# Optimization experiments

Hardware: AMD Instinct MI355X
Metric: run time of the kernel (lower is better)

The kernel has to match this reference:

```python
import jax, jax.numpy as jnp
import numpy as np

TOP_K = 8
NORM_TOPK_PROB = True


def setup_inputs() -> dict:
    key = jax.random.key(0)
    k1, k2 = jax.random.split(key)
    T, H, E = 16384, 4096, 64  # tokens, hidden_dim, num_experts
    hidden_states = jax.random.normal(k1, (T, H), dtype=jnp.float32)
    weight = jax.random.normal(k2, (E, H), dtype=jnp.float32) * 0.02
    return {"hidden_states": hidden_states, "weight": weight}


def reference(hidden_states, weight):
    H = weight.shape[1]
    x = hidden_states.reshape(-1, H)                      # [T, H]
    router_logits = jnp.einsum("th,eh->te", x, weight)    # [T, E]
    routing_weights = jax.nn.softmax(router_logits.astype(jnp.float32), axis=-1)
    router_top_value, router_indices = jax.lax.top_k(routing_weights, TOP_K)  # [T, k]
    if NORM_TOPK_PROB:
        router_top_value = router_top_value / jnp.sum(router_top_value, axis=-1, keepdims=True)
    router_scores = router_top_value.astype(routing_weights.dtype)
    return router_logits, router_scores, router_indices
```

## Files before the change

### kernel.cpp

```cpp
#include <hip/hip_runtime.h>
#include <math.h>

#define T_TOK  16384
#define HID    4096
#define NEXP   64
#define KSPLIT 4
#define KRANGE (HID / KSPLIT)
#define NCHUNK (KRANGE / 32)

typedef __attribute__((ext_vector_type(8))) short short8;
typedef __attribute__((ext_vector_type(4))) float float4v;

#define PART_ELEMS ((size_t)KSPLIT * T_TOK * NEXP)
#define WHALF      ((size_t)NEXP * HID)

__device__ __forceinline__ unsigned short rne_bf16(float f) {
  unsigned u = __float_as_uint(f);
  unsigned r = u + 0x7FFFu + ((u >> 16) & 1u);
  return (unsigned short)(r >> 16);
}
__device__ __forceinline__ float bf16_f(unsigned short h) {
  return __uint_as_float(((unsigned)h) << 16);
}

__global__ void w_convert3(const float* __restrict__ w,
                           unsigned short* __restrict__ wh,
                           unsigned short* __restrict__ wm,
                           unsigned short* __restrict__ wl) {
  int t = blockIdx.x * 256 + threadIdx.x;
#pragma unroll
  for (int j = 0; j < 4; ++j) {
    int idx = t + j * 65536;
    float f = w[idx];
    unsigned short h = rne_bf16(f);
    float r1 = f - bf16_f(h);
    unsigned short m = rne_bf16(r1);
    float r2 = r1 - bf16_f(m);
    wh[idx] = h; wm[idx] = m; wl[idx] = rne_bf16(r2);
  }
}

__global__ __launch_bounds__(256, 2)
void router_gemm(const float* __restrict__ x,
                 const unsigned short* __restrict__ wh,
                 const unsigned short* __restrict__ wm,
                 const unsigned short* __restrict__ wl,
                 float* __restrict__ partial) {
  const int lane = threadIdx.x & 63;
  const int wid  = threadIdx.x >> 6;
  const int W    = blockIdx.x * 4 + wid;
  const int ks   = W & (KSPLIT - 1);
  const int t0   = (W >> 2) * 32;
  const int r    = lane & 15;
  const int q    = lane >> 4;
  const int k0   = ks * KRANGE + q * 8;

  const float* pa0 = x + (size_t)(t0 + r) * HID + k0;
  const float* pa1 = pa0 + (size_t)16 * HID;
  const unsigned short* pb[3];
  pb[0] = wh + (size_t)r * HID + k0;
  pb[1] = wm + (size_t)r * HID + k0;
  pb[2] = wl + (size_t)r * HID + k0;

  float4v acc[2][4];
#pragma unroll
  for (int m = 0; m < 2; ++m)
#pragma unroll
    for (int n = 0; n < 4; ++n) acc[m][n] = (float4v)(0.f);

  float4 araw[4][2][2];
  short8 ah[2], am_[2], al[2];
  short8 Bb[2][2][3];

#define LOADA(buf, c) do {                                                   \
    const int _o = (c) * 32;                                                 \
    araw[buf][0][0] = *(const float4*)(pa0 + _o);                            \
    araw[buf][0][1] = *(const float4*)(pa0 + _o + 4);                        \
    araw[buf][1][0] = *(const float4*)(pa1 + _o);                            \
    araw[buf][1][1] = *(const float4*)(pa1 + _o + 4);                        \
  } while (0)

#define LOADB(half, c) do {                                                  \
    const int _o = (c) * 32;                                                 \
    _Pragma("unroll")                                                        \
    for (int _nl = 0; _nl < 2; ++_nl) {                                      \
      const size_t _nb = (size_t)((half) * 2 + _nl) * 16 * HID + _o;         \
      _Pragma("unroll")                                                      \
      for (int _s = 0; _s < 3; ++_s)                                         \
        Bb[half][_nl][_s] = *(const short8*)(pb[_s] + _nb);                  \
    }                                                                        \
  } while (0)

#define SPLITA(buf) do {                                                     \
    _Pragma("unroll")                                                        \
    for (int _m = 0; _m < 2; ++_m) {                                         \
      const float4 _v0 = araw[buf][_m][0], _v1 = araw[buf][_m][1];           \
      float _f[8] = {_v0.x,_v0.y,_v0.z,_v0.w,_v1.x,_v1.y,_v1.z,_v1.w};       \
      _Pragma("unroll")                                                      \
      for (int _j = 0; _j < 8; ++_j) {                                       \
        unsigned short _h = rne_bf16(_f[_j]);                                \
        float _r1 = _f[_j] - bf16_f(_h);                                     \
        unsigned short _mm = rne_bf16(_r1);                                  \
        float _r2 = _r1 - bf16_f(_mm);                                       \
        ah[_m][_j] = (short)_h; am_[_m][_j] = (short)_mm;                    \
        al[_m][_j] = (short)rne_bf16(_r2);                                   \
      }                                                                      \
    }                                                                        \
  } while (0)

#define MFMAH(half) do {                                                     \
    _Pragma("unroll")                                                        \
    for (int _nl = 0; _nl < 2; ++_nl) {                                      \
      const int _n = (half) * 2 + _nl;                                       \
      const short8 _BH = Bb[half][_nl][0];                                   \
      const short8 _BM = Bb[half][_nl][1];                                   \
      const short8 _BL = Bb[half][_nl][2];                                   \
      _Pragma("unroll")                                                      \
      for (int _m = 0; _m < 2; ++_m) {                                       \
        float4v _a = acc[_m][_n];                                            \
        _a = __builtin_amdgcn_mfma_f32_16x16x32_bf16(al[_m],  _BH, _a,0,0,0);\
        _a = __builtin_amdgcn_mfma_f32_16x16x32_bf16(ah[_m],  _BL, _a,0,0,0);\
        _a = __builtin_amdgcn_mfma_f32_16x16x32_bf16(am_[_m], _BM, _a,0,0,0);\
        _a = __builtin_amdgcn_mfma_f32_16x16x32_bf16(am_[_m], _BH, _a,0,0,0);\
        _a = __builtin_amdgcn_mfma_f32_16x16x32_bf16(ah[_m],  _BM, _a,0,0,0);\
        _a = __builtin_amdgcn_mfma_f32_16x16x32_bf16(ah[_m],  _BH, _a,0,0,0);\
        acc[_m][_n] = _a;                                                    \
      }                                                                      \
    }                                                                        \
  } while (0)

  LOADA(0, 0); LOADA(1, 1);
  LOADB(0, 0);
  for (int cc = 0; cc < NCHUNK; cc += 4) {
    if (cc + 2 < NCHUNK) LOADA(2, cc + 2);
    SPLITA(0); LOADB(1, cc);     MFMAH(0);
    LOADB(0, cc + 1);            MFMAH(1);

    if (cc + 3 < NCHUNK) LOADA(3, cc + 3);
    SPLITA(1); LOADB(1, cc + 1); MFMAH(0);
    LOADB(0, cc + 2);            MFMAH(1);

    if (cc + 4 < NCHUNK) LOADA(0, cc + 4);
    SPLITA(2); LOADB(1, cc + 2); MFMAH(0);
    LOADB(0, cc + 3);            MFMAH(1);

    if (cc + 5 < NCHUNK) LOADA(1, cc + 5);
    SPLITA(3); LOADB(1, cc + 3); MFMAH(0);
    if (cc + 4 < NCHUNK) LOADB(0, cc + 4);
    MFMAH(1);
  }
#undef LOADA
#undef LOADB
#undef SPLITA
#undef MFMAH

  float* po = partial + ((size_t)ks * T_TOK + t0) * NEXP;
#pragma unroll
  for (int m = 0; m < 2; ++m)
#pragma unroll
    for (int n = 0; n < 4; ++n)
#pragma unroll
      for (int rr = 0; rr < 4; ++rr)
        po[(size_t)(m * 16 + q * 4 + rr) * NEXP + n * 16 + r] = acc[m][n][rr];
}

__global__ __launch_bounds__(256)
void router_topk(const float* __restrict__ partial,
                 float* __restrict__ logits_out,
                 float* __restrict__ scores_out,
                 float* __restrict__ idx_out) {
  const int lane = threadIdx.x & 63;
  const int wid  = threadIdx.x >> 6;
  const int t    = blockIdx.x * 4 + wid;

  float ps[KSPLIT];
#pragma unroll
  for (int s = 0; s < KSPLIT; ++s)
    ps[s] = partial[((size_t)s * T_TOK + t) * NEXP + lane];
  float l = (ps[0] + ps[1]) + (ps[2] + ps[3]);
  logits_out[(size_t)t * NEXP + lane] = l;

  float m = l;
#pragma unroll
  for (int off = 32; off >= 1; off >>= 1)
    m = fmaxf(m, __shfl_xor(m, off, 64));
  float p = __expf(l - m);

  float v = l;
  float myscore = 0.f, myidx = 0.f, ssum = 0.f;
#pragma unroll
  for (int k = 0; k < 8; ++k) {
    float bv = v; int bi = lane;
#pragma unroll
    for (int off = 32; off >= 1; off >>= 1) {
      float ov = __shfl_xor(bv, off, 64);
      int   oi = __shfl_xor(bi, off, 64);
      if (ov > bv || (ov == bv && oi < bi)) { bv = ov; bi = oi; }
    }
    float pw = __shfl(p, bi, 64);
    ssum += pw;
    if (lane == k)  { myscore = pw; myidx = (float)bi; }
    if (lane == bi) v = -INFINITY;
  }
  if (lane < 8) {
    scores_out[(size_t)t * 8 + lane] = myscore / ssum;
    idx_out[(size_t)t * 8 + lane]    = myidx;
  }
}

extern "C" void kernel_launch(void* const* d_in, const int* in_sizes, int n_in,
                              void* d_out, int out_size, void* d_ws, size_t ws_size,
                              hipStream_t stream) {
  const float* x = (const float*)d_in[0];
  const float* w = (const float*)d_in[1];
  float* out    = (float*)d_out;
  float* logits = out;
  float* scores = out + (size_t)T_TOK * NEXP;
  float* idxo   = scores + (size_t)T_TOK * 8;

  float* partial = (float*)d_ws;
  unsigned short* wh = (unsigned short*)((char*)d_ws + PART_ELEMS * sizeof(float));
  unsigned short* wm = wh + WHALF;
  unsigned short* wl = wm + WHALF;

  hipLaunchKernelGGL(w_convert3, dim3(256), dim3(256), 0, stream, w, wh, wm, wl);
  hipLaunchKernelGGL(router_gemm, dim3(2048 / 4), dim3(256), 0, stream,
                     x, wh, wm, wl, partial);
  hipLaunchKernelGGL(router_topk, dim3(T_TOK / 4), dim3(256), 0, stream,
                     partial, logits, scores, idxo);
}
```

Baseline: 457.7 us.

## Halve per-wave token tile to 16 rows and raise GEMM occupancy

Each wave now computes 16 tokens instead of 32. That halves the accumulator and A-operand register footprint, allows launch bounds of 4 blocks per CU, and doubles the grid. The A prefetch is also deepened to three chunks ahead, and B loads are reordered ahead of the split step. The cost is that each B fragment (the three bf16 weight splits) is reused across only one M-tile instead of two, so weight-load traffic per flop doubles.

```diff
diff --git a/kernel.cpp b/kernel.cpp
--- a/kernel.cpp
+++ b/kernel.cpp
@@ -40,7 +40,7 @@
   }
 }
 
-__global__ __launch_bounds__(256, 2)
+__global__ __launch_bounds__(256, 4)
 void router_gemm(const float* __restrict__ x,
                  const unsigned short* __restrict__ wh,
                  const unsigned short* __restrict__ wm,
@@ -50,34 +50,29 @@
   const int wid  = threadIdx.x >> 6;
   const int W    = blockIdx.x * 4 + wid;
   const int ks   = W & (KSPLIT - 1);
-  const int t0   = (W >> 2) * 32;
+  const int t0   = (W >> 2) * 16;
   const int r    = lane & 15;
   const int q    = lane >> 4;
   const int k0   = ks * KRANGE + q * 8;
 
   const float* pa0 = x + (size_t)(t0 + r) * HID + k0;
-  const float* pa1 = pa0 + (size_t)16 * HID;
   const unsigned short* pb[3];
   pb[0] = wh + (size_t)r * HID + k0;
   pb[1] = wm + (size_t)r * HID + k0;
   pb[2] = wl + (size_t)r * HID + k0;
 
-  float4v acc[2][4];
-#pragma unroll
-  for (int m = 0; m < 2; ++m)
-#pragma unroll
-    for (int n = 0; n < 4; ++n) acc[m][n] = (float4v)(0.f);
-
-  float4 araw[4][2][2];
-  short8 ah[2], am_[2], al[2];
+  float4v acc[4];
+#pragma unroll
+  for (int n = 0; n < 4; ++n) acc[n] = (float4v)(0.f);
+
+  float4 araw[4][2];
+  short8 ah, am_, al;
   short8 Bb[2][2][3];
 
 #define LOADA(buf, c) do {                                                   \
     const int _o = (c) * 32;                                                 \
-    araw[buf][0][0] = *(const float4*)(pa0 + _o);                            \
-    araw[buf][0][1] = *(const float4*)(pa0 + _o + 4);                        \
-    araw[buf][1][0] = *(const float4*)(pa1 + _o);                            \
-    araw[buf][1][1] = *(const float4*)(pa1 + _o + 4);                        \
+    araw[buf][0] = *(const float4*)(pa0 + _o);                               \
+    araw[buf][1] = *(const float4*)(pa0 + _o + 4);                           \
   } while (0)
 
 #define LOADB(half, c) do {                                                  \
@@ -92,19 +87,16 @@
   } while (0)
 
 #define SPLITA(buf) do {                                                     \
+    const float4 _v0 = araw[buf][0], _v1 = araw[buf][1];                     \
+    float _f[8] = {_v0.x,_v0.y,_v0.z,_v0.w,_v1.x,_v1.y,_v1.z,_v1.w};         \
     _Pragma("unroll")                                                        \
-    for (int _m = 0; _m < 2; ++_m) {                                         \
-      const float4 _v0 = araw[buf][_m][0], _v1 = araw[buf][_m][1];           \
-      float _f[8] = {_v0.x,_v0.y,_v0.z,_v0.w,_v1.x,_v1.y,_v1.z,_v1.w};       \
-      _Pragma("unroll")                                                      \
-      for (int _j = 0; _j < 8; ++_j) {                                       \
-        unsigned short _h = rne_bf16(_f[_j]);                                \
-        float _r1 = _f[_j] - bf16_f(_h);                                     \
-        unsigned short _mm = rne_bf16(_r1);                                  \
-        float _r2 = _r1 - bf16_f(_mm);                                       \
-        ah[_m][_j] = (short)_h; am_[_m][_j] = (short)_mm;                    \
-        al[_m][_j] = (short)rne_bf16(_r2);                                   \
-      }                                                                      \
+    for (int _j = 0; _j < 8; ++_j) {                                         \
+      unsigned short _h = rne_bf16(_f[_j]);                                  \
+      float _r1 = _f[_j] - bf16_f(_h);                                       \
+      unsigned short _mm = rne_bf16(_r1);                                    \
+      float _r2 = _r1 - bf16_f(_mm);                                         \
+      ah[_j] = (short)_h; am_[_j] = (short)_mm;                              \
+      al[_j] = (short)rne_bf16(_r2);                                         \
     }                                                                        \
   } while (0)
 
@@ -115,39 +107,47 @@
       const short8 _BH = Bb[half][_nl][0];                                   \
       const short8 _BM = Bb[half][_nl][1];                                   \
       const short8 _BL = Bb[half][_nl][2];                                   \
-      _Pragma("unroll")                                                      \
-      for (int _m = 0; _m < 2; ++_m) {                                       \
-        float4v _a = acc[_m][_n];                                            \
-        _a = __builtin_amdgcn_mfma_f32_16x16x32_bf16(al[_m],  _BH, _a,0,0,0);\
-        _a = __builtin_amdgcn_mfma_f32_16x16x32_bf16(ah[_m],  _BL, _a,0,0,0);\
-        _a = __builtin_amdgcn_mfma_f32_16x16x32_bf16(am_[_m], _BM, _a,0,0,0);\
-        _a = __builtin_amdgcn_mfma_f32_16x16x32_bf16(am_[_m], _BH, _a,0,0,0);\
-        _a = __builtin_amdgcn_mfma_f32_16x16x32_bf16(ah[_m],  _BM, _a,0,0,0);\
-        _a = __builtin_amdgcn_mfma_f32_16x16x32_bf16(ah[_m],  _BH, _a,0,0,0);\
-        acc[_m][_n] = _a;                                                    \
-      }                                                                      \
+      float4v _a = acc[_n];                                                  \
+      _a = __builtin_amdgcn_mfma_f32_16x16x32_bf16(al,  _BH, _a, 0, 0, 0);   \
+      _a = __builtin_amdgcn_mfma_f32_16x16x32_bf16(ah,  _BL, _a, 0, 0, 0);   \
+      _a = __builtin_amdgcn_mfma_f32_16x16x32_bf16(am_, _BM, _a, 0, 0, 0);   \
+      _a = __builtin_amdgcn_mfma_f32_16x16x32_bf16(am_, _BH, _a, 0, 0, 0);   \
+      _a = __builtin_amdgcn_mfma_f32_16x16x32_bf16(ah,  _BM, _a, 0, 0, 0);   \
+      _a = __builtin_amdgcn_mfma_f32_16x16x32_bf16(ah,  _BH, _a, 0, 0, 0);   \
+      acc[_n] = _a;                                                          \
     }                                                                        \
   } while (0)
 
-  LOADA(0, 0); LOADA(1, 1);
+  LOADA(0, 0); LOADA(1, 1); LOADA(2, 2);
   LOADB(0, 0);
   for (int cc = 0; cc < NCHUNK; cc += 4) {
-    if (cc + 2 < NCHUNK) LOADA(2, cc + 2);
-    SPLITA(0); LOADB(1, cc);     MFMAH(0);
-    LOADB(0, cc + 1);            MFMAH(1);
-
+    LOADB(1, cc);
+    SPLITA(0);
+    MFMAH(0);
+    LOADB(0, cc + 1);
+    MFMAH(1);
     if (cc + 3 < NCHUNK) LOADA(3, cc + 3);
-    SPLITA(1); LOADB(1, cc + 1); MFMAH(0);
-    LOADB(0, cc + 2);            MFMAH(1);
-
+
+    LOADB(1, cc + 1);
+    SPLITA(1);
+    MFMAH(0);
+    LOADB(0, cc + 2);
+    MFMAH(1);
     if (cc + 4 < NCHUNK) LOADA(0, cc + 4);
-    SPLITA(2); LOADB(1, cc + 2); MFMAH(0);
-    LOADB(0, cc + 3);            MFMAH(1);
-
+
+    LOADB(1, cc + 2);
+    SPLITA(2);
+    MFMAH(0);
+    LOADB(0, cc + 3);
+    MFMAH(1);
     if (cc + 5 < NCHUNK) LOADA(1, cc + 5);
-    SPLITA(3); LOADB(1, cc + 3); MFMAH(0);
+
+    LOADB(1, cc + 3);
+    SPLITA(3);
+    MFMAH(0);
     if (cc + 4 < NCHUNK) LOADB(0, cc + 4);
     MFMAH(1);
+    if (cc + 6 < NCHUNK) LOADA(2, cc + 6);
   }
 #undef LOADA
 #undef LOADB
@@ -156,12 +156,10 @@
 
   float* po = partial + ((size_t)ks * T_TOK + t0) * NEXP;
 #pragma unroll
-  for (int m = 0; m < 2; ++m)
-#pragma unroll
-    for (int n = 0; n < 4; ++n)
-#pragma unroll
-      for (int rr = 0; rr < 4; ++rr)
-        po[(size_t)(m * 16 + q * 4 + rr) * NEXP + n * 16 + r] = acc[m][n][rr];
+  for (int n = 0; n < 4; ++n)
+#pragma unroll
+    for (int rr = 0; rr < 4; ++rr)
+      po[(size_t)(q * 4 + rr) * NEXP + n * 16 + r] = acc[n][rr];
 }
 
 __global__ __launch_bounds__(256)
@@ -224,7 +222,7 @@
   unsigned short* wl = wm + WHALF;
 
   hipLaunchKernelGGL(w_convert3, dim3(256), dim3(256), 0, stream, w, wh, wm, wl);
-  hipLaunchKernelGGL(router_gemm, dim3(2048 / 4), dim3(256), 0, stream,
+  hipLaunchKernelGGL(router_gemm, dim3(4096 / 4), dim3(256), 0, stream,
                      x, wh, wm, wl, partial);
   hipLaunchKernelGGL(router_topk, dim3(T_TOK / 4), dim3(256), 0, stream,
                      partial, logits, scores, idxo);
```

Result: slower. 541.8 us (+18.4%).

## Stage weight tiles in LDS via direct global-to-LDS loads; per-thread top-k

Applied to the files above, without the earlier changes.

The GEMM now has all four waves in a block share the same K-slice. The three bf16 weight splits are staged into a double-buffered, XOR-swizzled LDS tile with global_load_lds, which replaces per-wave redundant global loads of B, and barriers with explicit vmcnt waits pipeline the staging. The top-k kernel is rewritten so each thread handles one token: logits are transposed through padded LDS and an 8-entry insertion sort runs in registers instead of wave-wide shuffle reductions. The risks are the added barrier sync, LDS footprint, and register pressure from the 64-float row per thread.

```diff
diff --git a/kernel.cpp b/kernel.cpp
--- a/kernel.cpp
+++ b/kernel.cpp
@@ -6,7 +6,6 @@
 #define NEXP   64
 #define KSPLIT 4
 #define KRANGE (HID / KSPLIT)
-#define NCHUNK (KRANGE / 32)
 
 typedef __attribute__((ext_vector_type(8))) short short8;
 typedef __attribute__((ext_vector_type(4))) float float4v;
@@ -43,24 +42,35 @@
 __global__ __launch_bounds__(256, 2)
 void router_gemm(const float* __restrict__ x,
                  const unsigned short* __restrict__ wh,
-                 const unsigned short* __restrict__ wm,
-                 const unsigned short* __restrict__ wl,
                  float* __restrict__ partial) {
-  const int lane = threadIdx.x & 63;
-  const int wid  = threadIdx.x >> 6;
-  const int W    = blockIdx.x * 4 + wid;
-  const int ks   = W & (KSPLIT - 1);
-  const int t0   = (W >> 2) * 32;
+  __shared__ float4 ldsb4[3072];
+  char* ldsc = (char*)ldsb4;
+  const int tid  = threadIdx.x;
+  const int lane = tid & 63;
+  const int wid  = tid >> 6;
+  const int b    = blockIdx.x;
+  const int ks   = b & (KSPLIT - 1);
+  const int t0   = (b >> 2) * 128 + wid * 32;
   const int r    = lane & 15;
   const int q    = lane >> 4;
-  const int k0   = ks * KRANGE + q * 8;
-
-  const float* pa0 = x + (size_t)(t0 + r) * HID + k0;
+
+  const float* pa0 = x + (size_t)(t0 + r) * HID + ks * KRANGE + q * 8;
   const float* pa1 = pa0 + (size_t)16 * HID;
-  const unsigned short* pb[3];
-  pb[0] = wh + (size_t)r * HID + k0;
-  pb[1] = wm + (size_t)r * HID + k0;
-  pb[2] = wl + (size_t)r * HID + k0;
+
+  const char* sp[6];
+#pragma unroll
+  for (int it = 0; it < 6; ++it) {
+    int o  = it * 4096 + tid * 16;
+    int s  = o >> 13;
+    int e  = (o >> 7) & 63;
+    int kb = (o & 127) ^ ((e & 7) << 4);
+    sp[it] = (const char*)wh + (size_t)s * 524288 + (size_t)e * 8192
+           + ks * 2048 + kb;
+  }
+
+  const int swz = (r & 7) << 4;
+  const int a0 = r * 128 + ((q * 16) ^ swz);
+  const int a1 = r * 128 + ((q * 16 + 64) ^ swz);
 
   float4v acc[2][4];
 #pragma unroll
@@ -70,31 +80,31 @@
 
   float4 araw[4][2][2];
   short8 ah[2], am_[2], al[2];
-  short8 Bb[2][2][3];
-
-#define LOADA(buf, c) do {                                                   \
+
+#define STAGE(buf) do {                                                      \
+    _Pragma("unroll")                                                        \
+    for (int _it = 0; _it < 6; ++_it) {                                      \
+      __builtin_amdgcn_global_load_lds(                                      \
+        (const __attribute__((address_space(1))) unsigned int*)sp[_it],      \
+        (__attribute__((address_space(3))) unsigned int*)                    \
+          (ldsc + (buf) * 24576 + _it * 4096 + wid * 1024),                  \
+        16, 0, 0);                                                           \
+      sp[_it] += 128;                                                        \
+    }                                                                        \
+  } while (0)
+
+#define LOADA(slot, c) do {                                                  \
     const int _o = (c) * 32;                                                 \
-    araw[buf][0][0] = *(const float4*)(pa0 + _o);                            \
-    araw[buf][0][1] = *(const float4*)(pa0 + _o + 4);                        \
-    araw[buf][1][0] = *(const float4*)(pa1 + _o);                            \
-    araw[buf][1][1] = *(const float4*)(pa1 + _o + 4);                        \
-  } while (0)
-
-#define LOADB(half, c) do {                                                  \
-    const int _o = (c) * 32;                                                 \
-    _Pragma("unroll")                                                        \
-    for (int _nl = 0; _nl < 2; ++_nl) {                                      \
-      const size_t _nb = (size_t)((half) * 2 + _nl) * 16 * HID + _o;         \
-      _Pragma("unroll")                                                      \
-      for (int _s = 0; _s < 3; ++_s)                                         \
-        Bb[half][_nl][_s] = *(const short8*)(pb[_s] + _nb);                  \
-    }                                                                        \
-  } while (0)
-
-#define SPLITA(buf) do {                                                     \
+    araw[slot][0][0] = *(const float4*)(pa0 + _o);                           \
+    araw[slot][0][1] = *(const float4*)(pa0 + _o + 4);                       \
+    araw[slot][1][0] = *(const float4*)(pa1 + _o);                           \
+    araw[slot][1][1] = *(const float4*)(pa1 + _o + 4);                       \
+  } while (0)
+
+#define SPLITA(slot) do {                                                    \
     _Pragma("unroll")                                                        \
     for (int _m = 0; _m < 2; ++_m) {                                         \
-      const float4 _v0 = araw[buf][_m][0], _v1 = araw[buf][_m][1];           \
+      const float4 _v0 = araw[slot][_m][0], _v1 = araw[slot][_m][1];         \
       float _f[8] = {_v0.x,_v0.y,_v0.z,_v0.w,_v1.x,_v1.y,_v1.z,_v1.w};       \
       _Pragma("unroll")                                                      \
       for (int _j = 0; _j < 8; ++_j) {                                       \
@@ -108,51 +118,68 @@
     }                                                                        \
   } while (0)
 
-#define MFMAH(half) do {                                                     \
+#define CHUNK(buf, cl) do {                                                  \
     _Pragma("unroll")                                                        \
-    for (int _nl = 0; _nl < 2; ++_nl) {                                      \
-      const int _n = (half) * 2 + _nl;                                       \
-      const short8 _BH = Bb[half][_nl][0];                                   \
-      const short8 _BM = Bb[half][_nl][1];                                   \
-      const short8 _BL = Bb[half][_nl][2];                                   \
+    for (int _h = 0; _h < 2; ++_h) {                                         \
+      short8 _B[2][3];                                                       \
       _Pragma("unroll")                                                      \
-      for (int _m = 0; _m < 2; ++_m) {                                       \
-        float4v _a = acc[_m][_n];                                            \
-        _a = __builtin_amdgcn_mfma_f32_16x16x32_bf16(al[_m],  _BH, _a,0,0,0);\
-        _a = __builtin_amdgcn_mfma_f32_16x16x32_bf16(ah[_m],  _BL, _a,0,0,0);\
-        _a = __builtin_amdgcn_mfma_f32_16x16x32_bf16(am_[_m], _BM, _a,0,0,0);\
-        _a = __builtin_amdgcn_mfma_f32_16x16x32_bf16(am_[_m], _BH, _a,0,0,0);\
-        _a = __builtin_amdgcn_mfma_f32_16x16x32_bf16(ah[_m],  _BM, _a,0,0,0);\
-        _a = __builtin_amdgcn_mfma_f32_16x16x32_bf16(ah[_m],  _BH, _a,0,0,0);\
-        acc[_m][_n] = _a;                                                    \
+      for (int _nl = 0; _nl < 2; ++_nl)                                      \
+        _Pragma("unroll")                                                    \
+        for (int _s = 0; _s < 3; ++_s)                                       \
+          _B[_nl][_s] = *(const short8*)(ldsc + (buf) * 24576 + _s * 8192    \
+              + (_h * 2 + _nl) * 2048 + ((cl) ? a1 : a0));                   \
+      _Pragma("unroll")                                                      \
+      for (int _nl = 0; _nl < 2; ++_nl) {                                    \
+        const int _n = _h * 2 + _nl;                                         \
+        const short8 _BH = _B[_nl][0], _BM = _B[_nl][1], _BL = _B[_nl][2];   \
+        _Pragma("unroll")                                                    \
+        for (int _m = 0; _m < 2; ++_m) {                                     \
+          float4v _a = acc[_m][_n];                                          \
+          _a = __builtin_amdgcn_mfma_f32_16x16x32_bf16(al[_m],  _BH, _a,0,0,0);\
+          _a = __builtin_amdgcn_mfma_f32_16x16x32_bf16(ah[_m],  _BL, _a,0,0,0);\
+          _a = __builtin_amdgcn_mfma_f32_16x16x32_bf16(am_[_m], _BM, _a,0,0,0);\
+          _a = __builtin_amdgcn_mfma_f32_16x16x32_bf16(am_[_m], _BH, _a,0,0,0);\
+          _a = __builtin_amdgcn_mfma_f32_16x16x32_bf16(ah[_m],  _BM, _a,0,0,0);\
+          _a = __builtin_amdgcn_mfma_f32_16x16x32_bf16(ah[_m],  _BH, _a,0,0,0);\
+          acc[_m][_n] = _a;                                                  \
+        }                                                                    \
       }                                                                      \
     }                                                                        \
   } while (0)
 
-  LOADA(0, 0); LOADA(1, 1);
-  LOADB(0, 0);
-  for (int cc = 0; cc < NCHUNK; cc += 4) {
-    if (cc + 2 < NCHUNK) LOADA(2, cc + 2);
-    SPLITA(0); LOADB(1, cc);     MFMAH(0);
-    LOADB(0, cc + 1);            MFMAH(1);
-
-    if (cc + 3 < NCHUNK) LOADA(3, cc + 3);
-    SPLITA(1); LOADB(1, cc + 1); MFMAH(0);
-    LOADB(0, cc + 2);            MFMAH(1);
-
-    if (cc + 4 < NCHUNK) LOADA(0, cc + 4);
-    SPLITA(2); LOADB(1, cc + 2); MFMAH(0);
-    LOADB(0, cc + 3);            MFMAH(1);
-
-    if (cc + 5 < NCHUNK) LOADA(1, cc + 5);
-    SPLITA(3); LOADB(1, cc + 3); MFMAH(0);
-    if (cc + 4 < NCHUNK) LOADB(0, cc + 4);
-    MFMAH(1);
-  }
+  STAGE(0);
+  LOADA(0, 0); LOADA(1, 1); LOADA(2, 2); LOADA(3, 3);
+  asm volatile("s_waitcnt vmcnt(16)" ::: "memory");
+  __builtin_amdgcn_s_barrier();
+
+  for (int gg = 0; gg < 7; ++gg) {
+    const int c0 = gg * 4;
+    STAGE(1);
+    SPLITA(0); CHUNK(0, 0);
+    LOADA(0, c0 + 4);
+    SPLITA(1); CHUNK(0, 1);
+    LOADA(1, c0 + 5);
+    asm volatile("s_waitcnt vmcnt(8)" ::: "memory");
+    __builtin_amdgcn_s_barrier();
+    STAGE(0);
+    SPLITA(2); CHUNK(1, 0);
+    LOADA(2, c0 + 6);
+    SPLITA(3); CHUNK(1, 1);
+    LOADA(3, c0 + 7);
+    asm volatile("s_waitcnt vmcnt(8)" ::: "memory");
+    __builtin_amdgcn_s_barrier();
+  }
+  STAGE(1);
+  SPLITA(0); CHUNK(0, 0);
+  SPLITA(1); CHUNK(0, 1);
+  asm volatile("s_waitcnt vmcnt(0)" ::: "memory");
+  __builtin_amdgcn_s_barrier();
+  SPLITA(2); CHUNK(1, 0);
+  SPLITA(3); CHUNK(1, 1);
+#undef STAGE
 #undef LOADA
-#undef LOADB
 #undef SPLITA
-#undef MFMAH
+#undef CHUNK
 
   float* po = partial + ((size_t)ks * T_TOK + t0) * NEXP;
 #pragma unroll
@@ -164,47 +191,63 @@
         po[(size_t)(m * 16 + q * 4 + rr) * NEXP + n * 16 + r] = acc[m][n][rr];
 }
 
-__global__ __launch_bounds__(256)
+__global__ __launch_bounds__(64)
 void router_topk(const float* __restrict__ partial,
                  float* __restrict__ logits_out,
                  float* __restrict__ scores_out,
                  float* __restrict__ idx_out) {
-  const int lane = threadIdx.x & 63;
-  const int wid  = threadIdx.x >> 6;
-  const int t    = blockIdx.x * 4 + wid;
-
-  float ps[KSPLIT];
-#pragma unroll
-  for (int s = 0; s < KSPLIT; ++s)
-    ps[s] = partial[((size_t)s * T_TOK + t) * NEXP + lane];
-  float l = (ps[0] + ps[1]) + (ps[2] + ps[3]);
-  logits_out[(size_t)t * NEXP + lane] = l;
-
-  float m = l;
-#pragma unroll
-  for (int off = 32; off >= 1; off >>= 1)
-    m = fmaxf(m, __shfl_xor(m, off, 64));
-  float p = __expf(l - m);
-
-  float v = l;
-  float myscore = 0.f, myidx = 0.f, ssum = 0.f;
-#pragma unroll
-  for (int k = 0; k < 8; ++k) {
-    float bv = v; int bi = lane;
-#pragma unroll
-    for (int off = 32; off >= 1; off >>= 1) {
-      float ov = __shfl_xor(bv, off, 64);
-      int   oi = __shfl_xor(bi, off, 64);
-      if (ov > bv || (ov == bv && oi < bi)) { bv = ov; bi = oi; }
+  __shared__ float lt[64 * 68];
+  const int lane = threadIdx.x;
+  const int t0   = blockIdx.x * 64;
+
+#pragma unroll
+  for (int tt = 0; tt < 64; ++tt) {
+    const size_t tb = (size_t)(t0 + tt) * NEXP + lane;
+    float a0 = partial[tb];
+    float a1 = partial[(size_t)1 * T_TOK * NEXP + tb];
+    float a2 = partial[(size_t)2 * T_TOK * NEXP + tb];
+    float a3 = partial[(size_t)3 * T_TOK * NEXP + tb];
+    float l  = (a0 + a1) + (a2 + a3);
+    logits_out[(size_t)(t0 + tt) * NEXP + lane] = l;
+    lt[tt * 68 + lane] = l;
+  }
+  __syncthreads();
+
+  float rowf[64];
+#pragma unroll
+  for (int i = 0; i < 16; ++i) {
+    float4 v = *(const float4*)&lt[lane * 68 + i * 4];
+    rowf[i * 4 + 0] = v.x; rowf[i * 4 + 1] = v.y;
+    rowf[i * 4 + 2] = v.z; rowf[i * 4 + 3] = v.w;
+  }
+
+  float tv[8]; int ti[8];
+#pragma unroll
+  for (int k2 = 0; k2 < 8; ++k2) { tv[k2] = -INFINITY; ti[k2] = 0; }
+#pragma unroll
+  for (int j = 0; j < 64; ++j) {
+    float v = rowf[j]; int id = j;
+#pragma unroll
+    for (int k2 = 0; k2 < 8; ++k2) {
+      bool g2 = v > tv[k2];
+      float nv = g2 ? v : tv[k2];
+      int   ni = g2 ? id : ti[k2];
+      float ov = g2 ? tv[k2] : v;
+      int   oi = g2 ? ti[k2] : id;
+      tv[k2] = nv; ti[k2] = ni; v = ov; id = oi;
     }
-    float pw = __shfl(p, bi, 64);
-    ssum += pw;
-    if (lane == k)  { myscore = pw; myidx = (float)bi; }
-    if (lane == bi) v = -INFINITY;
-  }
-  if (lane < 8) {
-    scores_out[(size_t)t * 8 + lane] = myscore / ssum;
-    idx_out[(size_t)t * 8 + lane]    = myidx;
+  }
+
+  const float mx = tv[0];
+  float p[8]; float ssum = 0.f;
+#pragma unroll
+  for (int k2 = 0; k2 < 8; ++k2) { p[k2] = __expf(tv[k2] - mx); ssum += p[k2]; }
+  const float inv = 1.0f / ssum;
+  const size_t t = (size_t)(t0 + lane);
+#pragma unroll
+  for (int k2 = 0; k2 < 8; ++k2) {
+    scores_out[t * 8 + k2] = p[k2] * inv;
+    idx_out[t * 8 + k2]    = (float)ti[k2];
   }
 }
 
@@ -224,8 +267,8 @@
   unsigned short* wl = wm + WHALF;
 
   hipLaunchKernelGGL(w_convert3, dim3(256), dim3(256), 0, stream, w, wh, wm, wl);
-  hipLaunchKernelGGL(router_gemm, dim3(2048 / 4), dim3(256), 0, stream,
-                     x, wh, wm, wl, partial);
-  hipLaunchKernelGGL(router_topk, dim3(T_TOK / 4), dim3(256), 0, stream,
+  hipLaunchKernelGGL(router_gemm, dim3(512), dim3(256), 0, stream,
+                     x, wh, partial);
+  hipLaunchKernelGGL(router_topk, dim3(T_TOK / 64), dim3(64), 0, stream,
                      partial, logits, scores, idxo);
 }
```

Result: faster. 395.8 us (-13.5%).
